# Kernel tuning notes

Hardware: AMD Instinct MI355X
Metric: run time of the kernel (lower is better)

## Reference

```python
import jax, jax.numpy as jnp
import numpy as np

B, S, D, E, K = 4, 2048, 1024, 8, 2
EPS, W_THRES, TEMP = 1e-4, 0.1, 1.0


def setup_inputs() -> dict:
    key = jax.random.key(0)
    k1, k2, k3, k4, k5 = jax.random.split(key, 5)
    x = jax.random.normal(k1, (B, S, D), dtype=jnp.float32)
    gate_W = jax.random.normal(k2, (D, E), dtype=jnp.float32) * 0.02
    gate_b = jnp.zeros((E,), dtype=jnp.float32)
    expert_W = jax.random.normal(k3, (E, D, D), dtype=jnp.float32) * 0.02
    expert_b = jnp.zeros((E, D), dtype=jnp.float32)
    return {"x": x, "gate_W": gate_W, "gate_b": gate_b,
            "expert_W": expert_W, "expert_b": expert_b}


def reference(x, gate_W, gate_b, expert_W, expert_b):
    # Gating: linear -> temperature -> clamp-min(eps) -> softmax
    scores = jnp.maximum((x @ gate_W + gate_b) / TEMP, EPS)      # [B,S,E]
    p = jax.nn.softmax(scores, axis=-1)                           # [B,S,E]
    _, topk_idx = jax.lax.top_k(p, K)                             # [B,S,K]
    # boolean membership mask of selected experts
    topk_mask = jax.nn.one_hot(topk_idx, E, dtype=p.dtype).sum(-2) > 0  # [B,S,E]
    # weights: clamp-min(weight_thres), normalized by detached sum over selected
    w = jnp.maximum(p, W_THRES)                                   # [B,S,E]
    w_gather = jnp.take_along_axis(w, topk_idx, axis=-1)          # [B,S,K]
    total = jax.lax.stop_gradient(w_gather.sum(-1, keepdims=True))
    w = w / total
    comb = jnp.where(topk_mask, w, jnp.zeros_like(w))             # [B,S,E]
    # Dense equivalent of gather/expert/scatter loop (E small): each expert
    # is Linear(D, D); masked combine weights zero out unselected experts.
    y = jnp.einsum('bsd,edf->bsef', x, expert_W) + expert_b       # [B,S,E,D]
    out = jnp.einsum('bsef,bse->bsf', y, comb) / K                # [B,S,D]
    return out
```

## Files before the change

### kernel.cpp

```cpp
#include <hip/hip_runtime.h>
#include <hip/hip_fp16.h>
#include <stdint.h>

#define TOK 8192
#define DIM 1024
#define NE 8
#define NTILE 136

typedef short bf16x8 __attribute__((ext_vector_type(8)));
typedef float f32x4 __attribute__((ext_vector_type(4)));

__device__ __forceinline__ unsigned short f2bf(float f) {
  unsigned int u = __float_as_uint(f);
  u += 0x7FFFu + ((u >> 16) & 1u);
  return (unsigned short)(u >> 16);
}

__device__ __forceinline__ void gl_lds16(const void* g, void* l) {
  __builtin_amdgcn_global_load_lds(
      (__attribute__((address_space(1))) unsigned int*)(g),
      (__attribute__((address_space(3))) unsigned int*)(l), 16, 0, 0);
}

__global__ __launch_bounds__(256) void gate_kernel(
    const float* __restrict__ x, const float* __restrict__ gW,
    const float* __restrict__ gb, unsigned short* __restrict__ xb,
    int* __restrict__ eSel, float* __restrict__ wSel, int* __restrict__ cnt)
{
  if (blockIdx.x == 0 && threadIdx.x < NE) cnt[threadIdx.x] = 0;

  __shared__ float gWs[NE * DIM];
#pragma unroll
  for (int h = 0; h < 8; ++h) {
    const int m = threadIdx.x + h * 256;
    float4 v = ((const float4*)gW)[m];
    const int d = m >> 1, e0 = (m & 1) * 4;
    gWs[(e0 + 0) * DIM + d] = v.x;
    gWs[(e0 + 1) * DIM + d] = v.y;
    gWs[(e0 + 2) * DIM + d] = v.z;
    gWs[(e0 + 3) * DIM + d] = v.w;
  }
  __syncthreads();

  const int wave = threadIdx.x >> 6;
  const int lane = threadIdx.x & 63;
  const int t = blockIdx.x * 4 + wave;
  const float4* xrow = (const float4*)(x + (size_t)t * DIM);
  ushort4* xbrow = (ushort4*)(xb + (size_t)t * DIM);

  double acc[NE];
#pragma unroll
  for (int e = 0; e < NE; ++e) acc[e] = 0.0;

#pragma unroll
  for (int i = 0; i < 4; ++i) {
    const int j = i * 64 + lane;
    float4 v = xrow[j];
    ushort4 pk;
    pk.x = f2bf(v.x); pk.y = f2bf(v.y); pk.z = f2bf(v.z); pk.w = f2bf(v.w);
    xbrow[j] = pk;
#pragma unroll
    for (int e = 0; e < NE; ++e) {
      float4 gv = *(const float4*)&gWs[e * DIM + j * 4];
      acc[e] += (double)v.x * (double)gv.x + (double)v.y * (double)gv.y
              + (double)v.z * (double)gv.z + (double)v.w * (double)gv.w;
    }
  }
#pragma unroll
  for (int off = 32; off > 0; off >>= 1) {
#pragma unroll
    for (int e = 0; e < NE; ++e)
      acc[e] += __shfl_xor(acc[e], off, 64);
  }

  if (lane == 0) {
    double s[NE];
#pragma unroll
    for (int e = 0; e < NE; ++e) {
      s[e] = acc[e] + (double)gb[e];
      if (s[e] < 1e-4) s[e] = 1e-4;
    }
    int e0 = 0;
    for (int e = 1; e < NE; ++e) if (s[e] > s[e0]) e0 = e;
    int e1 = (e0 == 0) ? 1 : 0;
    for (int e = 0; e < NE; ++e) if (e != e0 && s[e] > s[e1]) e1 = e;
    float m = (float)s[e0];
    float Z = 0.f, pf[NE];
#pragma unroll
    for (int e = 0; e < NE; ++e) { pf[e] = __expf((float)s[e] - m); Z += pf[e]; }
    float w0 = pf[e0] / Z; if (w0 < 0.1f) w0 = 0.1f;
    float w1 = pf[e1] / Z; if (w1 < 0.1f) w1 = 0.1f;
    const float inv = 0.5f / (w0 + w1);
    eSel[t * 2 + 0] = e0;
    eSel[t * 2 + 1] = e1;
    wSel[t * 2 + 0] = w0 * inv;
    wSel[t * 2 + 1] = w1 * inv;
  }
}

__global__ __launch_bounds__(256) void scatter_kernel(
    const int* __restrict__ eSel, const float* __restrict__ wSel,
    int* __restrict__ cnt, int* __restrict__ listTok, float* __restrict__ listW)
{
  __shared__ int lcnt[NE];
  __shared__ int base[NE];
  const int tid = threadIdx.x;
  if (tid < NE) lcnt[tid] = 0;
  __syncthreads();

  const int t = blockIdx.x * 256 + tid;
  const int e0 = eSel[t * 2 + 0];
  const int e1 = eSel[t * 2 + 1];
  const float w0 = wSel[t * 2 + 0];
  const float w1 = wSel[t * 2 + 1];
  const int l0 = atomicAdd(&lcnt[e0], 1);
  const int l1 = atomicAdd(&lcnt[e1], 1);
  __syncthreads();
  if (tid < NE) base[tid] = atomicAdd(&cnt[tid], lcnt[tid]);
  __syncthreads();

  const int p0 = base[e0] + l0;
  listTok[e0 * TOK + p0] = t * 2 + 0;
  listW [e0 * TOK + p0] = w0;
  const int p1 = base[e1] + l1;
  listTok[e1 * TOK + p1] = t * 2 + 1;
  listW [e1 * TOK + p1] = w1;
}

__global__ __launch_bounds__(256) void transpose_w(
    const float* __restrict__ W, unsigned short* __restrict__ Wt)
{
  __shared__ float t2[64 * 33];
  const int e  = blockIdx.x >> 5;
  const int fb = blockIdx.x & 31;
  const int f0 = fb * 32;
  const int tid = threadIdx.x;
  const float* Wb = W + (size_t)e * DIM * DIM + f0;
  unsigned short* Ob = Wt + ((size_t)e * DIM + f0) * DIM;

  for (int kc = 0; kc < 16; ++kc) {
    const int d0 = kc * 64;
    __syncthreads();
#pragma unroll
    for (int h = 0; h < 8; ++h) {
      const int idx = tid + h * 256;
      t2[(idx >> 5) * 33 + (idx & 31)] = Wb[(size_t)(d0 + (idx >> 5)) * DIM + (idx & 31)];
    }
    __syncthreads();
#pragma unroll
    for (int h = 0; h < 8; ++h) {
      const int o = tid + h * 256;
      Ob[(size_t)(o >> 6) * DIM + d0 + (o & 63)] = f2bf(t2[(o & 63) * 33 + (o >> 6)]);
    }
  }
}

__global__ __launch_bounds__(256) void moe_gemm(
    const unsigned short* __restrict__ xb, const unsigned short* __restrict__ Wt,
    const float* __restrict__ eb, const int* __restrict__ cnt,
    const int* __restrict__ listTok, const float* __restrict__ listW,
    __half* __restrict__ yslot)
{
  const int dId = blockIdx.x % NTILE;
  const int cT  = blockIdx.x / NTILE;
  int e = -1, r0 = 0, rows = 0, accT = 0;
#pragma unroll
  for (int ee = 0; ee < NE; ++ee) {
    const int c = cnt[ee];
    const int nt = (c + 127) >> 7;
    if (dId >= accT && dId < accT + nt) {
      e = ee; r0 = (dId - accT) * 128;
      rows = c - r0; if (rows > 128) rows = 128;
    }
    accT += nt;
  }
  if (e < 0) return;

  __shared__ __align__(16) unsigned short As[2][128 * 32];
  __shared__ __align__(16) unsigned short Bs[2][128 * 32];
  __shared__ int   tid_s[128];
  __shared__ float w_s[128];

  const int tid = threadIdx.x;
  if (tid < 128) {
    if (tid < rows) {
      tid_s[tid] = listTok[e * TOK + r0 + tid];
      w_s[tid]   = listW [e * TOK + r0 + tid];
    } else {
      tid_s[tid] = 0;
      w_s[tid]   = 0.0f;
    }
  }
  __syncthreads();

  const int w    = tid >> 6;
  const int lane = tid & 63;
  const int qsrc = (lane & 3) ^ ((lane >> 3) & 3);
  const int rA0  = w * 32 + (lane >> 2);
  const int rA1  = rA0 + 16;
  const unsigned short* srcA0 = xb + (size_t)(tid_s[rA0] >> 1) * DIM + qsrc * 8;
  const unsigned short* srcA1 = xb + (size_t)(tid_s[rA1] >> 1) * DIM + qsrc * 8;
  const unsigned short* srcB0 = Wt + ((size_t)e * DIM + cT * 128 + rA0) * DIM + qsrc * 8;
  const unsigned short* srcB1 = Wt + ((size_t)e * DIM + cT * 128 + rA1) * DIM + qsrc * 8;

  const int wr = w >> 1, wc = w & 1;
  const int mrow = lane & 15;
  const int qg   = lane >> 4;
  const int qsA  = (qg ^ ((mrow >> 1) & 3)) * 8;

  f32x4 acc[4][4];
#pragma unroll
  for (int i = 0; i < 4; ++i)
#pragma unroll
    for (int j = 0; j < 4; ++j)
      acc[i][j] = {0.f, 0.f, 0.f, 0.f};

  gl_lds16(srcA0, &As[0][w * 1024]);
  gl_lds16(srcA1, &As[0][w * 1024 + 512]);
  gl_lds16(srcB0, &Bs[0][w * 1024]);
  gl_lds16(srcB1, &Bs[0][w * 1024 + 512]);

#pragma unroll 2
  for (int kc = 0; kc < DIM / 32; ++kc) {
    const int cur = kc & 1;
    __syncthreads();
    if (kc < DIM / 32 - 1) {
      const int k1 = (kc + 1) * 32;
      unsigned short* a = &As[cur ^ 1][w * 1024];
      unsigned short* b = &Bs[cur ^ 1][w * 1024];
      gl_lds16(srcA0 + k1, a);
      gl_lds16(srcA1 + k1, a + 512);
      gl_lds16(srcB0 + k1, b);
      gl_lds16(srcB1 + k1, b + 512);
    }
    bf16x8 af[4], bfr[4];
#pragma unroll
    for (int mt = 0; mt < 4; ++mt)
      af[mt] = *(const bf16x8*)&As[cur][(wr * 64 + mt * 16 + mrow) * 32 + qsA];
#pragma unroll
    for (int nt = 0; nt < 4; ++nt)
      bfr[nt] = *(const bf16x8*)&Bs[cur][(wc * 64 + nt * 16 + mrow) * 32 + qsA];
#pragma unroll
    for (int mt = 0; mt < 4; ++mt)
#pragma unroll
      for (int nt = 0; nt < 4; ++nt)
        acc[mt][nt] = __builtin_amdgcn_mfma_f32_16x16x32_bf16(
            af[mt], bfr[nt], acc[mt][nt], 0, 0, 0);
  }

  const int colBase = cT * 128 + wc * 64 + mrow;
  float bias[4];
#pragma unroll
  for (int nt = 0; nt < 4; ++nt)
    bias[nt] = eb[(size_t)e * DIM + colBase + nt * 16];
#pragma unroll
  for (int mt = 0; mt < 4; ++mt) {
#pragma unroll
    for (int r = 0; r < 4; ++r) {
      const int rloc = wr * 64 + mt * 16 + (lane >> 4) * 4 + r;
      if (rloc < rows) {
        const int tk    = tid_s[rloc];
        const float wgt = w_s[rloc];
        __half* dst = yslot + ((size_t)(tk & 1) * TOK + (size_t)(tk >> 1)) * DIM;
#pragma unroll
        for (int nt = 0; nt < 4; ++nt)
          dst[colBase + nt * 16] = __float2half(wgt * (acc[mt][nt][r] + bias[nt]));
      }
    }
  }
}

__global__ __launch_bounds__(256) void combine(
    const __half* __restrict__ y0, const __half* __restrict__ y1,
    float4* __restrict__ out)
{
  const size_t i = (size_t)blockIdx.x * 256 + threadIdx.x;
  const ushort4 ua = ((const ushort4*)y0)[i];
  const ushort4 ub = ((const ushort4*)y1)[i];
  const __half* ah = (const __half*)&ua;
  const __half* bh = (const __half*)&ub;
  float4 o;
  o.x = __half2float(ah[0]) + __half2float(bh[0]);
  o.y = __half2float(ah[1]) + __half2float(bh[1]);
  o.z = __half2float(ah[2]) + __half2float(bh[2]);
  o.w = __half2float(ah[3]) + __half2float(bh[3]);
  out[i] = o;
}

extern "C" void kernel_launch(void* const* d_in, const int* in_sizes, int n_in,
                              void* d_out, int out_size, void* d_ws, size_t ws_size,
                              hipStream_t stream)
{
  const float* x  = (const float*)d_in[0];
  const float* gW = (const float*)d_in[1];
  const float* gb = (const float*)d_in[2];
  const float* eW = (const float*)d_in[3];
  const float* eb = (const float*)d_in[4];
  float* out = (float*)d_out;

  char* p = (char*)d_ws;
  unsigned short* xb = (unsigned short*)p;  p += (size_t)TOK * DIM * 2;
  unsigned short* Wt = (unsigned short*)p;  p += (size_t)NE * DIM * DIM * 2;
  __half* yslot = (__half*)p;               p += (size_t)2 * TOK * DIM * 2;
  int* cnt = (int*)p;                       p += 256;
  int* listTok = (int*)p;                   p += (size_t)NE * TOK * 4;
  float* listW = (float*)p;                 p += (size_t)NE * TOK * 4;

  int*   eSel = (int*)yslot;
  float* wSel = (float*)((char*)yslot + TOK * 8);

  gate_kernel<<<TOK / 4, 256, 0, stream>>>(x, gW, gb, xb, eSel, wSel, cnt);
  scatter_kernel<<<TOK / 256, 256, 0, stream>>>(eSel, wSel, cnt, listTok, listW);
  transpose_w<<<NE * 32, 256, 0, stream>>>(eW, Wt);
  moe_gemm<<<NTILE * 8, 256, 0, stream>>>(xb, Wt, eb, cnt, listTok, listW, yslot);
  combine<<<TOK * DIM / 4 / 256, 256, 0, stream>>>(
      yslot, yslot + (size_t)TOK * DIM, (float4*)out);
}
```

Before: 211.9 us.

## Deepen GEMM LDS pipeline to four stages and retile weight transpose

The MoE GEMM moves from double to quad-buffered LDS. It prefetches three k-chunks ahead and uses explicit vmcnt waits with raw barriers in place of __syncthreads, aiming to hide global-load latency. Separately, the weight transpose kernel is retiled into 64x64 blocks across 2048 workgroups, with float4 loads and packed bf16 pair stores, for better parallelism and coalescing. The extra LDS doubles shared memory per GEMM block, which may lower occupancy, and the hand-counted waitcnts are fragile.

```diff
diff --git a/kernel.cpp b/kernel.cpp
--- a/kernel.cpp
+++ b/kernel.cpp
@@ -130,28 +130,32 @@
 __global__ __launch_bounds__(256) void transpose_w(
     const float* __restrict__ W, unsigned short* __restrict__ Wt)
 {
-  __shared__ float t2[64 * 33];
-  const int e  = blockIdx.x >> 5;
-  const int fb = blockIdx.x & 31;
-  const int f0 = fb * 32;
+  __shared__ float t2[64][65];
+  const int b  = blockIdx.x;
+  const int e  = b >> 8;
+  const int db = (b >> 4) & 15;
+  const int fb = b & 15;
+  const int d0 = db * 64, f0 = fb * 64;
   const int tid = threadIdx.x;
-  const float* Wb = W + (size_t)e * DIM * DIM + f0;
-  unsigned short* Ob = Wt + ((size_t)e * DIM + f0) * DIM;
-
-  for (int kc = 0; kc < 16; ++kc) {
-    const int d0 = kc * 64;
-    __syncthreads();
-#pragma unroll
-    for (int h = 0; h < 8; ++h) {
-      const int idx = tid + h * 256;
-      t2[(idx >> 5) * 33 + (idx & 31)] = Wb[(size_t)(d0 + (idx >> 5)) * DIM + (idx & 31)];
-    }
-    __syncthreads();
-#pragma unroll
-    for (int h = 0; h < 8; ++h) {
-      const int o = tid + h * 256;
-      Ob[(size_t)(o >> 6) * DIM + d0 + (o & 63)] = f2bf(t2[(o & 63) * 33 + (o >> 6)]);
-    }
+#pragma unroll
+  for (int h = 0; h < 4; ++h) {
+    const int idx = tid + h * 256;
+    const int r = idx >> 4, c4 = idx & 15;
+    float4 v = *(const float4*)&W[((size_t)e * DIM + d0 + r) * DIM + f0 + c4 * 4];
+    t2[r][c4 * 4 + 0] = v.x;
+    t2[r][c4 * 4 + 1] = v.y;
+    t2[r][c4 * 4 + 2] = v.z;
+    t2[r][c4 * 4 + 3] = v.w;
+  }
+  __syncthreads();
+#pragma unroll
+  for (int h = 0; h < 8; ++h) {
+    const int o = tid + h * 256;
+    const int f = o >> 5, k2 = (o & 31) * 2;
+    const unsigned int lo = f2bf(t2[k2][f]);
+    const unsigned int hi = f2bf(t2[k2 + 1][f]);
+    *(unsigned int*)&Wt[((size_t)e * DIM + f0 + f) * DIM + d0 + k2] =
+        lo | (hi << 16);
   }
 }
 
@@ -176,8 +180,8 @@
   }
   if (e < 0) return;
 
-  __shared__ __align__(16) unsigned short As[2][128 * 32];
-  __shared__ __align__(16) unsigned short Bs[2][128 * 32];
+  __shared__ __align__(16) unsigned short As[4][128 * 32];
+  __shared__ __align__(16) unsigned short Bs[4][128 * 32];
   __shared__ int   tid_s[128];
   __shared__ float w_s[128];
 
@@ -215,19 +219,25 @@
     for (int j = 0; j < 4; ++j)
       acc[i][j] = {0.f, 0.f, 0.f, 0.f};
 
-  gl_lds16(srcA0, &As[0][w * 1024]);
-  gl_lds16(srcA1, &As[0][w * 1024 + 512]);
-  gl_lds16(srcB0, &Bs[0][w * 1024]);
-  gl_lds16(srcB1, &Bs[0][w * 1024 + 512]);
-
-#pragma unroll 2
+#pragma unroll
+  for (int p = 0; p < 3; ++p) {
+    unsigned short* a = &As[p][w * 1024];
+    unsigned short* b = &Bs[p][w * 1024];
+    gl_lds16(srcA0 + p * 32, a);
+    gl_lds16(srcA1 + p * 32, a + 512);
+    gl_lds16(srcB0 + p * 32, b);
+    gl_lds16(srcB1 + p * 32, b + 512);
+  }
+  asm volatile("s_waitcnt vmcnt(8)" ::: "memory");
+  __builtin_amdgcn_s_barrier();
+
   for (int kc = 0; kc < DIM / 32; ++kc) {
-    const int cur = kc & 1;
-    __syncthreads();
-    if (kc < DIM / 32 - 1) {
-      const int k1 = (kc + 1) * 32;
-      unsigned short* a = &As[cur ^ 1][w * 1024];
-      unsigned short* b = &Bs[cur ^ 1][w * 1024];
+    const int cur = kc & 3;
+    if (kc + 3 < DIM / 32) {
+      const int k1 = (kc + 3) * 32;
+      const int nb = (kc + 3) & 3;
+      unsigned short* a = &As[nb][w * 1024];
+      unsigned short* b = &Bs[nb][w * 1024];
       gl_lds16(srcA0 + k1, a);
       gl_lds16(srcA1 + k1, a + 512);
       gl_lds16(srcB0 + k1, b);
@@ -246,6 +256,15 @@
       for (int nt = 0; nt < 4; ++nt)
         acc[mt][nt] = __builtin_amdgcn_mfma_f32_16x16x32_bf16(
             af[mt], bfr[nt], acc[mt][nt], 0, 0, 0);
+    if (kc < DIM / 32 - 1) {
+      if (kc < DIM / 32 - 3)
+        asm volatile("s_waitcnt vmcnt(8) lgkmcnt(0)" ::: "memory");
+      else if (kc == DIM / 32 - 3)
+        asm volatile("s_waitcnt vmcnt(4) lgkmcnt(0)" ::: "memory");
+      else
+        asm volatile("s_waitcnt vmcnt(0) lgkmcnt(0)" ::: "memory");
+      __builtin_amdgcn_s_barrier();
+    }
   }
 
   const int colBase = cT * 128 + wc * 64 + mrow;
@@ -311,7 +330,7 @@
 
   gate_kernel<<<TOK / 4, 256, 0, stream>>>(x, gW, gb, xb, eSel, wSel, cnt);
   scatter_kernel<<<TOK / 256, 256, 0, stream>>>(eSel, wSel, cnt, listTok, listW);
-  transpose_w<<<NE * 32, 256, 0, stream>>>(eW, Wt);
+  transpose_w<<<NE * 256, 256, 0, stream>>>(eW, Wt);
   moe_gemm<<<NTILE * 8, 256, 0, stream>>>(xb, Wt, eb, cnt, listTok, listW, yslot);
   combine<<<TOK * DIM / 4 / 256, 256, 0, stream>>>(
       yslot, yslot + (size_t)TOK * DIM, (float4*)out);
```

Measured after the change: 214.1 us. About the same (+1.0%).
